# Kernel optimization log

Hardware: AMD Instinct MI355X
Metric: run time of the kernel (lower is better)

Reference implementation:

```python
import jax, jax.numpy as jnp
import numpy as np

D = 1024
B, S = 4, 4096


def setup_inputs() -> dict:
    key = jax.random.key(0)
    ks = jax.random.split(key, 5)
    scale = 1.0 / np.sqrt(D)  # ~ torch Linear init magnitude
    return {
        "x": jax.random.normal(ks[0], (B, S, D), dtype=jnp.float32),
        "Wa": jax.random.normal(ks[1], (D, D), dtype=jnp.float32) * scale,
        "Wb": jax.random.normal(ks[2], (D, D), dtype=jnp.float32) * scale,
        "Wc": jax.random.normal(ks[3], (D, D), dtype=jnp.float32) * scale,
        "Wd": jax.random.normal(ks[4], (D, D), dtype=jnp.float32) * scale,
    }


def reference(x, Wa, Wb, Wc, Wd):
    # torch nn.Linear(bias=False): y = x @ W.T, W is [out, in]
    A = jax.nn.relu(jnp.einsum("bsd,ed->bse", x, Wa))
    Bm = jax.nn.relu(jnp.einsum("bsd,ed->bse", x, Wb))
    C = jax.nn.relu(jnp.einsum("bsd,ed->bse", x, Wc))
    cmp_matrix = jnp.einsum("bse,bte->bst", A, Bm)  # [B,S,S] unnormalized scores
    out = jnp.einsum("bst,bte->bse", cmp_matrix, C)
    return jax.nn.relu(jnp.einsum("bsd,ed->bse", out, Wd))
```

## Files before the change

### kernel.cpp

```cpp
#include <hip/hip_runtime.h>
#include <hip/hip_bf16.h>

#define D_ 1024
#define B_ 4
#define S_ 4096

typedef __attribute__((ext_vector_type(8))) short bf16x8;
typedef __attribute__((ext_vector_type(4))) float f32x4;
typedef __attribute__((ext_vector_type(4))) unsigned int u32x4;
typedef __attribute__((ext_vector_type(4))) unsigned short u16x4;

__device__ __forceinline__ unsigned short f2bf(float f) {
    unsigned int u = __builtin_bit_cast(unsigned int, f);
    u = u + 0x7fffu + ((u >> 16) & 1u);
    return (unsigned short)(u >> 16);
}
__device__ __forceinline__ unsigned int pk2(float a, float b) {
    return (unsigned int)f2bf(a) | ((unsigned int)f2bf(b) << 16);
}
__device__ __forceinline__ float bf2f(unsigned short h) {
    unsigned int u = ((unsigned int)h) << 16;
    return __builtin_bit_cast(float, u);
}
__device__ __forceinline__ void gload16(const void* g, void* l) {
    __builtin_amdgcn_global_load_lds(
        (const __attribute__((address_space(1))) void*)g,
        (__attribute__((address_space(3))) void*)l, 16, 0, 0);
}

__global__ __launch_bounds__(256)
void conv_bf16(const float* __restrict__ src, unsigned short* __restrict__ dst, int n8) {
    int i = blockIdx.x * blockDim.x + threadIdx.x;
    const int stride = gridDim.x * blockDim.x;
    for (; i < n8; i += stride) {
        f32x4 v0 = *(const f32x4*)(src + (size_t)i * 8);
        f32x4 v1 = *(const f32x4*)(src + (size_t)i * 8 + 4);
        u32x4 o;
        o[0] = pk2(v0[0], v0[1]);
        o[1] = pk2(v0[2], v0[3]);
        o[2] = pk2(v1[0], v1[1]);
        o[3] = pk2(v1[2], v1[3]);
        *(u32x4*)(dst + (size_t)i * 8) = o;
    }
}

__global__ __launch_bounds__(256)
void conv_bf16_w2(const float* __restrict__ s0, const float* __restrict__ s1,
                  unsigned short* __restrict__ d0, unsigned short* __restrict__ d1,
                  int n8_per) {
    int i = blockIdx.x * blockDim.x + threadIdx.x;
    const int stride = gridDim.x * blockDim.x;
    for (; i < 2 * n8_per; i += stride) {
        int w = i / n8_per;
        size_t j = (size_t)(i - w * n8_per) * 8;
        const float* s = w ? s1 : s0;
        unsigned short* d = w ? d1 : d0;
        f32x4 v0 = *(const f32x4*)(s + j);
        f32x4 v1 = *(const f32x4*)(s + j + 4);
        u32x4 o;
        o[0] = pk2(v0[0], v0[1]);
        o[1] = pk2(v0[2], v0[3]);
        o[2] = pk2(v1[0], v1[1]);
        o[3] = pk2(v1[2], v1[3]);
        *(u32x4*)(d + j) = o;
    }
}

__global__ __launch_bounds__(256)
void reduceN_bf16_inplace(unsigned short* __restrict__ P, int split, int n8_total) {
    int t = blockIdx.x * blockDim.x + threadIdx.x;
    const int stride = gridDim.x * blockDim.x;
    const int DD = D_ * D_;
    for (; t < n8_total; t += stride) {
        size_t idx = (size_t)t * 8;
        int b = (int)(idx / DD);
        size_t i = idx % DD;
        float s[8];
#pragma unroll
        for (int k = 0; k < 8; ++k) s[k] = 0.f;
        for (int seg = 0; seg < split; ++seg) {
            const unsigned short* p = P + (size_t)(b * split + seg) * DD + i;
            u16x4 v0 = *(const u16x4*)p;
            u16x4 v1 = *(const u16x4*)(p + 4);
#pragma unroll
            for (int k = 0; k < 4; ++k) { s[k] += bf2f(v0[k]); s[4 + k] += bf2f(v1[k]); }
        }
        u16x4 o0, o1;
#pragma unroll
        for (int k = 0; k < 4; ++k) { o0[k] = f2bf(s[k]); o1[k] = f2bf(s[4 + k]); }
        unsigned short* e = P + (size_t)(b * split) * DD + i;
        *(u16x4*)e = o0;
        *(u16x4*)(e + 4) = o1;
    }
}

#define BM 128
#define BN 128
#define BK 64
#define NTHR 256

template<bool OUT_F32, bool TRANS, bool RELU>
__global__ __launch_bounds__(NTHR)
void gemm_nt(const unsigned short* __restrict__ Ap, const unsigned short* __restrict__ Bp,
             void* __restrict__ Op, int M, int N, int K, int klen, int split,
             long long sA, long long sB, long long sO)
{
    __shared__ char lds_a[BM * BK * 2];
    __shared__ char lds_b[BN * BK * 2];

    const int tid   = threadIdx.x;
    const int bz    = blockIdx.z;
    const int batch = bz / split;
    const int k0    = (bz % split) * klen;
    const int bm    = blockIdx.y * BM;
    const int bn    = blockIdx.x * BN;

    const unsigned short* Abase = Ap + (size_t)batch * sA + (size_t)bm * K;
    const unsigned short* Bbase = Bp + (size_t)batch * sB + (size_t)bn * K;

    const int lane = tid & 63;
    const int wave = tid >> 6;
    const int wm   = (wave >> 1) * 64;
    const int wn   = (wave & 1) * 64;
    const int l16  = lane & 15;
    const int lhi  = lane >> 4;

    const int srow0 = wave * 32 + (lane >> 3);
    const int schnk = (lane & 7) ^ (lane >> 3);
    const char* gA0 = (const char*)(Abase + (size_t)srow0 * K) + schnk * 16;
    const char* gB0 = (const char*)(Bbase + (size_t)srow0 * K) + schnk * 16;
    char* lA0 = lds_a + wave * 4096;
    char* lB0 = lds_b + wave * 4096;

    f32x4 acc[4][4];
#pragma unroll
    for (int i = 0; i < 4; ++i)
#pragma unroll
        for (int j = 0; j < 4; ++j)
            acc[i][j] = (f32x4){0.f, 0.f, 0.f, 0.f};

    for (int kt = k0; kt < k0 + klen; kt += BK) {
#pragma unroll
        for (int p = 0; p < 4; ++p)
            gload16(gA0 + ((size_t)p * 8 * K + kt) * 2, lA0 + p * 1024);
#pragma unroll
        for (int p = 0; p < 4; ++p)
            gload16(gB0 + ((size_t)p * 8 * K + kt) * 2, lB0 + p * 1024);
        __syncthreads();
#pragma unroll
        for (int kk = 0; kk < BK / 32; ++kk) {
            bf16x8 af[4], bfr[4];
#pragma unroll
            for (int i = 0; i < 4; ++i) {
                int row = wm + i * 16 + l16;
                int byt = (row * 128 + kk * 64 + lhi * 16) ^ ((row & 7) << 4);
                af[i] = *(const bf16x8*)(lds_a + byt);
            }
#pragma unroll
            for (int j = 0; j < 4; ++j) {
                int row = wn + j * 16 + l16;
                int byt = (row * 128 + kk * 64 + lhi * 16) ^ ((row & 7) << 4);
                bfr[j] = *(const bf16x8*)(lds_b + byt);
            }
#pragma unroll
            for (int i = 0; i < 4; ++i)
#pragma unroll
                for (int j = 0; j < 4; ++j)
                    acc[i][j] = __builtin_amdgcn_mfma_f32_16x16x32_bf16(af[i], bfr[j], acc[i][j], 0, 0, 0);
        }
        __syncthreads();
    }

    const size_t obase = (size_t)bz * (size_t)sO;
    if constexpr (!TRANS) {
#pragma unroll
        for (int i = 0; i < 4; ++i) {
            const int m0 = bm + wm + i * 16 + lhi * 4;
#pragma unroll
            for (int j = 0; j < 4; ++j) {
                const int n = bn + wn + j * 16 + l16;
#pragma unroll
                for (int r = 0; r < 4; ++r) {
                    float v = acc[i][j][r];
                    if constexpr (RELU) v = fmaxf(v, 0.f);
                    size_t addr = obase + (size_t)(m0 + r) * N + n;
                    if constexpr (OUT_F32) ((float*)Op)[addr] = v;
                    else ((unsigned short*)Op)[addr] = f2bf(v);
                }
            }
        }
    } else {
#pragma unroll
        for (int i = 0; i < 4; ++i) {
            const int m0 = bm + wm + i * 16 + lhi * 4;
#pragma unroll
            for (int j = 0; j < 4; ++j) {
                const int n = bn + wn + j * 16 + l16;
                u16x4 h;
#pragma unroll
                for (int r = 0; r < 4; ++r) {
                    float v = acc[i][j][r];
                    if constexpr (RELU) v = fmaxf(v, 0.f);
                    h[r] = f2bf(v);
                }
                *(u16x4*)((unsigned short*)Op + obase + (size_t)n * M + m0) = h;
            }
        }
    }
}

#define CTILE 65536
#define CBOFF 32768

template<bool OUT_F32, bool TRANS, bool RELU>
__global__ __launch_bounds__(512, 2)
void gemm256(const unsigned short* __restrict__ Ap, const unsigned short* __restrict__ Bp,
             void* __restrict__ Op, int M, int N, int K, int klen, int split,
             long long sA, long long sB, long long sO)
{
    __shared__ char lds[131072];
    const int tid  = threadIdx.x;
    const int wave = tid >> 6;
    const int lane = tid & 63;

    const int gx = gridDim.x, gy = gridDim.y;
    const int f   = blockIdx.x + gx * (blockIdx.y + gy * blockIdx.z);
    const int nwg = gx * gy * (int)gridDim.z;
    const int s   = (f & 7) * (nwg >> 3) + (f >> 3);
    const int lx  = s % gx;
    const int lyz = s / gx;
    const int ly  = lyz % gy;
    const int lz  = lyz / gy;

    const int batch = lz / split;
    const int k0    = (lz % split) * klen;
    const int bm    = ly * 256;
    const int bn    = lx * 256;

    const int wm  = (wave >> 2) * 128;
    const int wn  = (wave & 3) * 64;
    const int l16 = lane & 15, lhi = lane >> 4;

    const unsigned short* Abase = Ap + (size_t)batch * sA + (size_t)bm * K;
    const unsigned short* Bbase = Bp + (size_t)batch * sB + (size_t)bn * K;
    const int srow  = lane >> 3;
    const int schnk = (lane & 7) ^ srow;
    const size_t K2 = (size_t)K * 2;
    const char* gA = (const char*)Abase + (size_t)srow * K2 + (size_t)schnk * 16 + (size_t)k0 * 2;
    const char* gB = (const char*)Bbase + (size_t)srow * K2 + (size_t)schnk * 16 + (size_t)k0 * 2;

    f32x4 acc[8][4];
#pragma unroll
    for (int i = 0; i < 8; ++i)
#pragma unroll
        for (int j = 0; j < 4; ++j)
            acc[i][j] = (f32x4){0.f, 0.f, 0.f, 0.f};

    bf16x8 a[4][2], b0[2][2], b1[2][2];

    auto stageA2 = [&](int c, int t, int h) {
#pragma unroll
        for (int p = 0; p < 2; ++p)
            gload16(gA + (size_t)t * 128 + (size_t)(h * 128 + wave * 16 + p * 8) * K2,
                    lds + c * CTILE + h * 16384 + wave * 2048 + p * 1024);
    };
    auto stageB2 = [&](int c, int t, int h) {
#pragma unroll
        for (int p = 0; p < 2; ++p)
            gload16(gB + (size_t)t * 128 + (size_t)(h * 128 + wave * 16 + p * 8) * K2,
                    lds + c * CTILE + CBOFF + h * 16384 + wave * 2048 + p * 1024);
    };
    auto ldA = [&](int c, int mh) {
#pragma unroll
        for (int i4 = 0; i4 < 4; ++i4)
#pragma unroll
            for (int kk = 0; kk < 2; ++kk) {
                int row = wm + mh * 64 + i4 * 16 + l16;
                int byt = (row * 128 + kk * 64 + lhi * 16) ^ ((row & 7) << 4);
                a[i4][kk] = *(const bf16x8*)(lds + c * CTILE + byt);
            }
    };
    auto ldB = [&](int c, int nh, bf16x8 (&bb)[2][2]) {
#pragma unroll
        for (int j2 = 0; j2 < 2; ++j2)
#pragma unroll
            for (int kk = 0; kk < 2; ++kk) {
                int row = wn + nh * 32 + j2 * 16 + l16;
                int byt = (row * 128 + kk * 64 + lhi * 16) ^ ((row & 7) << 4);
                bb[j2][kk] = *(const bf16x8*)(lds + c * CTILE + CBOFF + byt);
            }
    };
    auto mm = [&](int mh, int nh, bf16x8 (&bb)[2][2]) {
        __builtin_amdgcn_s_setprio(1);
#pragma unroll
        for (int i4 = 0; i4 < 4; ++i4)
#pragma unroll
            for (int j2 = 0; j2 < 2; ++j2)
#pragma unroll
                for (int kk = 0; kk < 2; ++kk)
                    acc[mh * 4 + i4][nh * 2 + j2] = __builtin_amdgcn_mfma_f32_16x16x32_bf16(
                        a[i4][kk], bb[j2][kk], acc[mh * 4 + i4][nh * 2 + j2], 0, 0, 0);
        __builtin_amdgcn_s_setprio(0);
    };

#define BAR()   __builtin_amdgcn_s_barrier()
#define LGKM0() asm volatile("s_waitcnt lgkmcnt(0)" ::: "memory")
#define LGKM8() asm volatile("s_waitcnt lgkmcnt(8)" ::: "memory")
#define VM4()   asm volatile("s_waitcnt vmcnt(4)" ::: "memory")
#define VM2()   asm volatile("s_waitcnt vmcnt(2)" ::: "memory")

    const int NT = klen / 64;
    stageA2(0, 0, 0); stageA2(0, 0, 1);
    stageB2(0, 0, 0); stageB2(0, 0, 1);
    stageA2(1, 1, 0);
    VM2();
    BAR();

    for (int itr = 0; itr < NT / 2; ++itr) {
        const int t1  = 2 * itr + 1;
        const int tp0 = (2 * itr + 2) % NT;
        const int tp1 = (2 * itr + 3) % NT;
        ldA(0, 0); ldB(0, 0, b0);
        stageB2(1, t1, 0); stageA2(1, t1, 1);
        LGKM8();
        BAR(); LGKM0(); mm(0, 0, b0); BAR();
        ldB(0, 1, b1);
        stageB2(1, t1, 1);
        BAR(); LGKM0(); mm(0, 1, b1); BAR();
        ldA(0, 1);
        stageB2(0, tp0, 0);
        BAR(); LGKM0(); mm(1, 0, b0); BAR();
        stageB2(0, tp0, 1);
        BAR(); mm(1, 1, b1); VM4(); BAR();
        ldA(1, 0); ldB(1, 0, b0);
        stageA2(0, tp0, 0);
        LGKM8();
        BAR(); LGKM0(); mm(0, 0, b0); BAR();
        ldB(1, 1, b1);
        stageA2(0, tp0, 1);
        BAR(); LGKM0(); mm(0, 1, b1); BAR();
        ldA(1, 1);
        BAR(); LGKM0(); mm(1, 0, b0); BAR();
        stageA2(1, tp1, 0);
        BAR(); mm(1, 1, b1); VM2(); BAR();
    }
    asm volatile("s_waitcnt vmcnt(0)" ::: "memory");

    const size_t obase = (size_t)lz * (size_t)sO;
    if constexpr (!TRANS) {
#pragma unroll
        for (int i = 0; i < 8; ++i) {
            const int m0 = bm + wm + i * 16 + lhi * 4;
#pragma unroll
            for (int j = 0; j < 4; ++j) {
                const int n = bn + wn + j * 16 + l16;
#pragma unroll
                for (int r = 0; r < 4; ++r) {
                    float v = acc[i][j][r];
                    if constexpr (RELU) v = fmaxf(v, 0.f);
                    size_t addr = obase + (size_t)(m0 + r) * N + n;
                    if constexpr (OUT_F32) ((float*)Op)[addr] = v;
                    else ((unsigned short*)Op)[addr] = f2bf(v);
                }
            }
        }
    } else {
#pragma unroll
        for (int i = 0; i < 8; ++i) {
            const int m0 = bm + wm + i * 16 + lhi * 4;
#pragma unroll
            for (int j = 0; j < 4; ++j) {
                const int n = bn + wn + j * 16 + l16;
                u16x4 h;
#pragma unroll
                for (int r = 0; r < 4; ++r) {
                    float v = acc[i][j][r];
                    if constexpr (RELU) v = fmaxf(v, 0.f);
                    h[r] = f2bf(v);
                }
                *(u16x4*)((unsigned short*)Op + obase + (size_t)n * M + m0) = h;
            }
        }
    }
#undef BAR
#undef LGKM0
#undef LGKM8
#undef VM4
#undef VM2
}

extern "C" void kernel_launch(void* const* d_in, const int* in_sizes, int n_in,
                              void* d_out, int out_size, void* d_ws, size_t ws_size,
                              hipStream_t stream) {
    (void)in_sizes; (void)n_in; (void)out_size; (void)ws_size;
    const float* x  = (const float*)d_in[0];
    const float* Wa = (const float*)d_in[1];
    const float* Wb = (const float*)d_in[2];
    const float* Wc = (const float*)d_in[3];
    const float* Wd = (const float*)d_in[4];

    const long long SD  = (long long)S_ * D_;
    const long long DD2 = (long long)D_ * D_;
    const size_t MB = 1024 * 1024;

    unsigned short* BC = (unsigned short*)d_ws;
    unsigned short* Ao = (unsigned short*)d_ws;
    unsigned short* Ft = (unsigned short*)((char*)d_ws + 32 * MB);
    char* ob = (char*)d_out;
    unsigned short* xb    = (unsigned short*)ob;
    unsigned short* Pp    = (unsigned short*)(ob + 32 * MB);
    unsigned short* Enorm = Pp;
    unsigned short* Wdb   = (unsigned short*)(ob + 34 * MB);
    unsigned short* Wab   = (unsigned short*)(ob + 36 * MB);
    unsigned short* Wbb   = (unsigned short*)(ob + 56 * MB);
    unsigned short* Wcb   = (unsigned short*)(ob + 58 * MB);

    dim3 blk256(256, 1, 1);
    dim3 blk512(512, 1, 1);
    dim3 gBC(2048 / 256, S_ / 256, B_);
    dim3 gE(D_ / 256, D_ / 256, B_ * 4);
    dim3 gS(D_ / 256, S_ / 256, B_);
    dim3 gF(D_ / BN, D_ / BM, B_);

    conv_bf16<<<2048, blk256, 0, stream>>>(x, xb, (B_ * S_ * D_) / 8);
    conv_bf16_w2<<<512, blk256, 0, stream>>>(Wb, Wc, Wbb, Wcb, (D_ * D_) / 8);
    gemm256<false, true,  true ><<<gBC, blk512, 0, stream>>>(xb, Wbb, BC, S_, 2048, D_, D_, 1, SD, 0, 2 * SD);
    gemm256<false, false, false><<<gE, blk512, 0, stream>>>(BC, BC + SD, Pp, D_, D_, S_, S_ / 4, 4, 2 * SD, 2 * SD, DD2);
    reduceN_bf16_inplace<<<2048, blk256, 0, stream>>>(Pp, 4, (B_ * D_ * D_) / 8);
    conv_bf16_w2<<<512, blk256, 0, stream>>>(Wd, Wa, Wdb, Wab, (D_ * D_) / 8);
    gemm_nt<false, true,  false><<<gF, blk256, 0, stream>>>(Enorm, Wdb, Ft, D_, D_, D_, D_, 1, 4 * DD2, 0, DD2);
    gemm256<false, false, true ><<<gS, blk512, 0, stream>>>(xb, Wab, Ao, S_, D_, D_, D_, 1, SD, 0, SD);
    gemm256<true,  false, true ><<<gS, blk512, 0, stream>>>(Ao, Ft, (float*)d_out, S_, D_, D_, D_, 1, SD, DD2, SD);
}
```

Before: 253.6 us.

## Restructure GEMM main loop to prefetch LDS fragments ahead of MFMA

Reorders the software pipeline in the bf16 GEMM main loop. LDS-to-register fragment loads for the next sub-tile are now issued right after each MFMA block, and the prologue stages both buffers' B tiles and primes the first fragments. This cuts the barriers per quarter-step from two to one and drops the extra waits before each MFMA block, so LDS reads and global staging overlap with compute. The risk is a hazard in the buffer reuse ordering or higher register pressure from keeping fragments live across barriers.

```diff
diff --git a/kernel.cpp b/kernel.cpp
--- a/kernel.cpp
+++ b/kernel.cpp
@@ -305,44 +305,45 @@
 
 #define BAR()   __builtin_amdgcn_s_barrier()
 #define LGKM0() asm volatile("s_waitcnt lgkmcnt(0)" ::: "memory")
-#define LGKM8() asm volatile("s_waitcnt lgkmcnt(8)" ::: "memory")
+#define VM2()   asm volatile("s_waitcnt vmcnt(2)" ::: "memory")
 #define VM4()   asm volatile("s_waitcnt vmcnt(4)" ::: "memory")
-#define VM2()   asm volatile("s_waitcnt vmcnt(2)" ::: "memory")
+#define VM6()   asm volatile("s_waitcnt vmcnt(6)" ::: "memory")
 
     const int NT = klen / 64;
-    stageA2(0, 0, 0); stageA2(0, 0, 1);
-    stageB2(0, 0, 0); stageB2(0, 0, 1);
-    stageA2(1, 1, 0);
-    VM2();
+    stageB2(0, 0, 0); stageB2(0, 0, 1); stageA2(0, 0, 0); stageA2(0, 0, 1);
+    stageB2(1, 1, 0); stageB2(1, 1, 1); stageA2(1, 1, 0);
+    VM6();
     BAR();
+    ldB(0, 0, b0); ldA(0, 0);
 
     for (int itr = 0; itr < NT / 2; ++itr) {
         const int t1  = 2 * itr + 1;
         const int tp0 = (2 * itr + 2) % NT;
         const int tp1 = (2 * itr + 3) % NT;
-        ldA(0, 0); ldB(0, 0, b0);
-        stageB2(1, t1, 0); stageA2(1, t1, 1);
-        LGKM8();
-        BAR(); LGKM0(); mm(0, 0, b0); BAR();
-        ldB(0, 1, b1);
-        stageB2(1, t1, 1);
-        BAR(); LGKM0(); mm(0, 1, b1); BAR();
-        ldA(0, 1);
-        stageB2(0, tp0, 0);
-        BAR(); LGKM0(); mm(1, 0, b0); BAR();
-        stageB2(0, tp0, 1);
-        BAR(); mm(1, 1, b1); VM4(); BAR();
-        ldA(1, 0); ldB(1, 0, b0);
-        stageA2(0, tp0, 0);
-        LGKM8();
-        BAR(); LGKM0(); mm(0, 0, b0); BAR();
-        ldB(1, 1, b1);
-        stageA2(0, tp0, 1);
-        BAR(); LGKM0(); mm(0, 1, b1); BAR();
-        ldA(1, 1);
-        BAR(); LGKM0(); mm(1, 0, b0); BAR();
-        stageA2(1, tp1, 0);
-        BAR(); mm(1, 1, b1); VM2(); BAR();
+        LGKM0(); mm(0, 0, b0);
+        ldB(0, 1, b1); stageA2(1, t1, 1);
+        BAR();
+        LGKM0(); mm(0, 1, b1);
+        ldA(0, 1); VM4();
+        BAR();
+        LGKM0(); mm(1, 0, b0);
+        ldB(1, 0, b0); stageB2(0, tp0, 0); VM2();
+        BAR();
+        LGKM0(); mm(1, 1, b1);
+        ldA(1, 0); stageB2(0, tp0, 1); stageA2(0, tp0, 0);
+        BAR();
+        LGKM0(); mm(0, 0, b0);
+        ldB(1, 1, b1); stageA2(0, tp0, 1);
+        BAR();
+        LGKM0(); mm(0, 1, b1);
+        ldA(1, 1); VM4();
+        BAR();
+        LGKM0(); mm(1, 0, b0);
+        ldB(0, 0, b0); stageB2(1, tp1, 0); VM2();
+        BAR();
+        LGKM0(); mm(1, 1, b1);
+        ldA(0, 0); stageB2(1, tp1, 1); stageA2(1, tp1, 0);
+        BAR();
     }
     asm volatile("s_waitcnt vmcnt(0)" ::: "memory");
 
@@ -384,9 +385,9 @@
     }
 #undef BAR
 #undef LGKM0
-#undef LGKM8
+#undef VM2
 #undef VM4
-#undef VM2
+#undef VM6
 }
 
 extern "C" void kernel_launch(void* const* d_in, const int* in_sizes, int n_in,
```

After: 243.4 us. 1.04x faster.
